# Kernel tuning notes

Measured on AMD Instinct MI355X. Metric: run time of the kernel, lower is better.

The kernel has to match this reference:

```python
import jax, jax.numpy as jnp
import numpy as np

B, T, C, H = 64, 256, 384, 6
HS = C // H  # 64


def _ln(x, w, b, eps=1e-5):
    m = jnp.mean(x, axis=-1, keepdims=True)
    v = jnp.mean((x - m) ** 2, axis=-1, keepdims=True)
    return (x - m) / jnp.sqrt(v + eps) * w + b


def setup_inputs() -> dict:
    key = jax.random.key(0)
    ks = jax.random.split(key, 18)
    sc = 0.02
    return {
        "x": jax.random.normal(ks[0], (B, T, C), jnp.float32),
        "ln1_w": jnp.ones((C,), jnp.float32),
        "ln1_b": jnp.zeros((C,), jnp.float32),
        # per-head Q/K/V linears stacked over the head axis: [H, C, HS]
        "Wq": jax.random.normal(ks[1], (H, C, HS), jnp.float32) * sc,
        "bq": jnp.zeros((H, HS), jnp.float32),
        "Wk": jax.random.normal(ks[2], (H, C, HS), jnp.float32) * sc,
        "bk": jnp.zeros((H, HS), jnp.float32),
        "Wv": jax.random.normal(ks[3], (H, C, HS), jnp.float32) * sc,
        "bv": jnp.zeros((H, HS), jnp.float32),
        "Wproj": jax.random.normal(ks[4], (C, C), jnp.float32) * sc,
        "bproj": jnp.zeros((C,), jnp.float32),
        "ln2_w": jnp.ones((C,), jnp.float32),
        "ln2_b": jnp.zeros((C,), jnp.float32),
        "W1": jax.random.normal(ks[5], (C, 4 * C), jnp.float32) * sc,
        "b1": jnp.zeros((4 * C,), jnp.float32),
        "W2": jax.random.normal(ks[6], (4 * C, C), jnp.float32) * sc,
        "b2": jnp.zeros((C,), jnp.float32),
    }


def reference(x, ln1_w, ln1_b, Wq, bq, Wk, bk, Wv, bv, Wproj, bproj,
              ln2_w, ln2_b, W1, b1, W2, b2):
    # --- pre-norm causal MHA (dropout = identity in eval) ---
    h = _ln(x, ln1_w, ln1_b)
    Q = jnp.einsum('btc,hcd->bhtd', h, Wq) + bq[None, :, None, :]
    K = jnp.einsum('btc,hcd->bhtd', h, Wk) + bk[None, :, None, :]
    V = jnp.einsum('btc,hcd->bhtd', h, Wv) + bv[None, :, None, :]
    scores = jnp.einsum('bhtd,bhsd->bhts', Q, K) * (HS ** -0.5)
    mask = jnp.tril(jnp.ones((x.shape[1], x.shape[1]), bool))
    scores = jnp.where(mask, scores, -jnp.inf)
    wei = jax.nn.softmax(scores, axis=-1)
    o = jnp.einsum('bhts,bhsd->bhtd', wei, V)
    # concat heads (same order as torch.cat over head list)
    o = o.transpose(0, 2, 1, 3).reshape(x.shape[0], x.shape[1], C)
    x1 = x + o @ Wproj + bproj
    # --- pre-norm FFN with exact (erf) GELU, matching torch default ---
    h2 = _ln(x1, ln2_w, ln2_b)
    f = jax.nn.gelu(h2 @ W1 + b1, approximate=False) @ W2 + b2
    return x1 + f
```

## Files before the change

### kernel.cpp

```cpp
#include <hip/hip_runtime.h>
#include <math.h>

constexpr int Bsz  = 64;
constexpr int Tseq = 256;
constexpr int Cdim = 384;
constexpr int Hh   = 6;
constexpr int HSd  = 64;
constexpr int Mrows = Bsz * Tseq;
constexpr int Cffn  = 4 * Cdim;
constexpr int Nqkv  = 3 * Cdim;

typedef __attribute__((ext_vector_type(8))) short short8;
typedef __attribute__((ext_vector_type(4))) float f32x4;

__device__ __forceinline__ ushort f2bf(float x) {
  union { float f; uint u; } a; a.f = x;
  uint r = a.u + 0x7fffu + ((a.u >> 16) & 1u);
  return (ushort)(r >> 16);
}
__device__ __forceinline__ float bf2f(ushort u) {
  union { uint u; float f; } a; a.u = ((uint)u) << 16;
  return a.f;
}

__device__ __forceinline__ float gelu_fast(float x) {
  float t = x * x;
  float u = x * fmaf(0.044715f, t, 1.0f);
  float e = fminf(1.5957691216f * u, 80.f);
  float z = __expf(e);
  return x * (z / (1.0f + z));
}

__global__ __launch_bounds__(256) void prep_kernel(
    const float* __restrict__ Wq, const float* __restrict__ Wk,
    const float* __restrict__ Wv, const float* __restrict__ Wproj,
    const float* __restrict__ W1, const float* __restrict__ W2,
    const float* __restrict__ bq, const float* __restrict__ bk,
    const float* __restrict__ bv,
    ushort* __restrict__ WqkvT, ushort* __restrict__ WprojT,
    ushort* __restrict__ W1T, ushort* __restrict__ W2T,
    float* __restrict__ bqkv) {
  const int bid = blockIdx.x;
  if (bid >= 1728) {
    int i = (bid - 1728) * 256 + threadIdx.x;
    if (i < Nqkv)
      bqkv[i] = (i < 384) ? bq[i] : (i < 768) ? bk[i - 384] : bv[i - 768];
    return;
  }
  const int tx = threadIdx.x & 31, ty = threadIdx.x >> 5;
  const float* src; ushort* dst; int R, S, r0, s0;
  if (bid < 432) {
    int which = bid / 144, rem = bid % 144;
    const float* W = (which == 0) ? Wq : (which == 1) ? Wk : Wv;
    int bz = rem / 24, t = rem % 24;
    R = 384; S = 64;
    src = W + (size_t)bz * R * S;
    dst = WqkvT + (size_t)which * 384 * 384 + (size_t)bz * R * S;
    r0 = (t >> 1) * 32; s0 = (t & 1) * 32;
  } else if (bid < 576) {
    int rem = bid - 432; R = 384; S = 384; src = Wproj; dst = WprojT;
    r0 = (rem / 12) * 32; s0 = (rem % 12) * 32;
  } else if (bid < 1152) {
    int rem = bid - 576; R = 384; S = 1536; src = W1; dst = W1T;
    r0 = (rem / 48) * 32; s0 = (rem % 48) * 32;
  } else {
    int rem = bid - 1152; R = 1536; S = 384; src = W2; dst = W2T;
    r0 = (rem / 12) * 32; s0 = (rem % 12) * 32;
  }
  __shared__ float t[32][33];
#pragma unroll
  for (int i = 0; i < 32; i += 8)
    t[ty + i][tx] = src[(size_t)(r0 + ty + i) * S + s0 + tx];
  __syncthreads();
#pragma unroll
  for (int i = 0; i < 32; i += 8)
    dst[(size_t)(s0 + ty + i) * R + r0 + tx] = f2bf(t[tx][ty + i]);
}

template <typename T>
__global__ __launch_bounds__(256) void ln_kernel(
    const T* __restrict__ x, const float* __restrict__ w,
    const float* __restrict__ b, ushort* __restrict__ out, int nrows) {
  int row  = blockIdx.x * 4 + (threadIdx.x >> 6);
  int lane = threadIdx.x & 63;
  if (row >= nrows) return;
  const T* xr = x + (size_t)row * Cdim;
  float v[6];
  float s = 0.f;
#pragma unroll
  for (int i = 0; i < 6; ++i) {
    if constexpr (sizeof(T) == 2) v[i] = bf2f(xr[lane + 64 * i]);
    else                          v[i] = xr[lane + 64 * i];
    s += v[i];
  }
#pragma unroll
  for (int off = 32; off > 0; off >>= 1) s += __shfl_xor(s, off, 64);
  float mean = s * (1.f / Cdim);
  float sq = 0.f;
#pragma unroll
  for (int i = 0; i < 6; ++i) { float d = v[i] - mean; sq += d * d; }
#pragma unroll
  for (int off = 32; off > 0; off >>= 1) sq += __shfl_xor(sq, off, 64);
  float rstd = rsqrtf(sq * (1.f / Cdim) + 1e-5f);
  ushort* orow = out + (size_t)row * Cdim;
#pragma unroll
  for (int i = 0; i < 6; ++i) {
    int c = lane + 64 * i;
    orow[c] = f2bf((v[i] - mean) * rstd * w[c] + b[c]);
  }
}

template <int EPI, int BN>
__global__ __launch_bounds__(256) void mfma_gemm(
    const ushort* __restrict__ A, const ushort* __restrict__ Bt,
    const float* __restrict__ bias, const void* __restrict__ res,
    void* __restrict__ Cout, void* __restrict__ C2, void* __restrict__ C3,
    int M, int N, int K) {
  constexpr int WC = BN / 2;
  constexpr int JN = WC / 16;
  constexpr int NB = BN / 32;
  __shared__ ushort Als[2 * 128 * 64];
  __shared__ ushort Bls[2 * BN * 64];
  const int tid = threadIdx.x;

  const int lid = blockIdx.y * gridDim.x + blockIdx.x;
  const int xcd = lid & 7, idx = lid >> 3;
  const int by = xcd * 16 + (idx & 15);
  const int bx = idx >> 4;
  const int m0 = by * 128, n0 = bx * BN;

  const int lane = tid & 63;
  const int w    = tid >> 6;
  const int wr   = (w >> 1) * 64;
  const int wc   = (w & 1) * WC;
  const int lm   = lane & 15;
  const int g    = lane >> 4;
  const int rq   = g * 4;

  const int wub = (tid & ~63) * 8;

  f32x4 acc[4][JN] = {};

  auto stage = [&](int k0, int bf) {
    ushort* Ab = Als + bf * (128 * 64);
    ushort* Bb = Bls + bf * (BN * 64);
#pragma unroll
    for (int q = 0; q < 4; ++q) {
      const int ci = tid + q * 256;
      const int row = ci >> 3;
      const int kc = ((ci & 7) ^ (row & 7)) * 8;
      const ushort* gA = A + (size_t)(m0 + row) * K + k0 + kc;
      __builtin_amdgcn_global_load_lds(
          (const __attribute__((address_space(1))) uint*)gA,
          (__attribute__((address_space(3))) uint*)(Ab + wub + q * 2048),
          16, 0, 0);
    }
#pragma unroll
    for (int q = 0; q < NB; ++q) {
      const int ci = tid + q * 256;
      const int row = ci >> 3;
      const int kc = ((ci & 7) ^ (row & 7)) * 8;
      const ushort* gB = Bt + (size_t)(n0 + row) * K + k0 + kc;
      __builtin_amdgcn_global_load_lds(
          (const __attribute__((address_space(1))) uint*)gB,
          (__attribute__((address_space(3))) uint*)(Bb + wub + q * 2048),
          16, 0, 0);
    }
  };

  const int nt = K >> 6;
  stage(0, 0);

  for (int t = 0, k0 = 0; t < nt; ++t, k0 += 64) {
    const int cur = t & 1;
    if (t + 1 < nt) {
      stage(k0 + 64, cur ^ 1);
      if constexpr (NB == 4)
        asm volatile("s_waitcnt vmcnt(8)" ::: "memory");
      else
        asm volatile("s_waitcnt vmcnt(6)" ::: "memory");
    } else {
      asm volatile("s_waitcnt vmcnt(0)" ::: "memory");
    }
    __builtin_amdgcn_sched_barrier(0);
    __builtin_amdgcn_s_barrier();
    __builtin_amdgcn_sched_barrier(0);

    const ushort* Ab = Als + cur * (128 * 64);
    const ushort* Bb = Bls + cur * (BN * 64);
#pragma unroll
    for (int half = 0; half < 2; ++half) {
      const int sl = ((half << 2) | g) ^ (lm & 7);
      short8 af[4], bfr[JN];
#pragma unroll
      for (int i = 0; i < 4; ++i)
        af[i] = *(const short8*)&Ab[(wr + i * 16 + lm) * 64 + sl * 8];
#pragma unroll
      for (int j = 0; j < JN; ++j)
        bfr[j] = *(const short8*)&Bb[(wc + j * 16 + lm) * 64 + sl * 8];
#pragma unroll
      for (int i = 0; i < 4; ++i)
#pragma unroll
        for (int j = 0; j < JN; ++j)
          acc[i][j] = __builtin_amdgcn_mfma_f32_16x16x32_bf16(af[i], bfr[j],
                                                              acc[i][j], 0, 0, 0);
    }

    asm volatile("s_waitcnt lgkmcnt(0)" ::: "memory");
    __builtin_amdgcn_sched_barrier(0);
    __builtin_amdgcn_s_barrier();
    __builtin_amdgcn_sched_barrier(0);
  }

  float bb[JN];
#pragma unroll
  for (int j = 0; j < JN; ++j) bb[j] = bias[n0 + wc + j * 16 + lm];

#pragma unroll
  for (int i = 0; i < 4; ++i) {
#pragma unroll
    for (int r = 0; r < 4; ++r) {
      const int row = m0 + wr + i * 16 + rq + r;
      if (EPI == 1) {
        const float* resrow = (const float*)res + (size_t)row * N + n0 + wc;
        ushort* crow = (ushort*)Cout + (size_t)row * N + n0 + wc;
#pragma unroll
        for (int j = 0; j < JN; ++j) {
          float rv = __builtin_nontemporal_load(resrow + j * 16 + lm);
          crow[j * 16 + lm] = f2bf(acc[i][j][r] + bb[j] + rv);
        }
      } else if (EPI == 4) {
        const ushort* resrow = (const ushort*)res + (size_t)row * N + n0 + wc;
        float* crow = (float*)Cout + (size_t)row * N + n0 + wc;
#pragma unroll
        for (int j = 0; j < JN; ++j)
          crow[j * 16 + lm] = acc[i][j][r] + bb[j] + bf2f(resrow[j * 16 + lm]);
      } else if (EPI == 3) {
        const int bb_ = row >> 8, tt = row & 255;
#pragma unroll
        for (int j = 0; j < JN; ++j) {
          const int colb = n0 + wc + j * 16;
          const int sec = colb / 384, cc = colb % 384;
          const int hh = cc >> 6, db = (cc & 63) + lm;
          ushort* dstp = (sec == 0) ? (ushort*)Cout
                       : (sec == 1) ? (ushort*)C2 : (ushort*)C3;
          dstp[((size_t)(bb_ * Hh + hh) * Tseq + tt) * HSd + db] =
              f2bf(acc[i][j][r] + bb[j]);
        }
      } else {
        ushort* crow = (ushort*)Cout + (size_t)row * N + n0 + wc;
#pragma unroll
        for (int j = 0; j < JN; ++j)
          crow[j * 16 + lm] = f2bf(gelu_fast(acc[i][j][r] + bb[j]));
      }
    }
  }
}

__global__ __launch_bounds__(256) void attn_kernel(
    const ushort* __restrict__ Qb, const ushort* __restrict__ Kb,
    const ushort* __restrict__ Vb, ushort* __restrict__ Oc) {
  __shared__ ushort Ks[64 * 72];
  __shared__ ushort Vt[64 * 72];
  __shared__ ushort Pl[4][16 * 72];
  const int bh = blockIdx.x, qt = blockIdx.y;
  const int b = bh / Hh, h = bh % Hh;
  const int tid = threadIdx.x;
  const int w = tid >> 6, lane = tid & 63;
  const int g = lane >> 4, n16 = lane & 15;

  const ushort* qrow = Qb + ((size_t)bh * Tseq + qt * 64 + w * 16 + n16) * HSd;
  short8 qf0 = *(const short8*)(qrow + g * 8);
  short8 qf1 = *(const short8*)(qrow + 32 + g * 8);

  f32x4 oacc[4] = {};
  float m_r[4], l_r[4];
#pragma unroll
  for (int r = 0; r < 4; ++r) { m_r[r] = -1e30f; l_r[r] = 0.f; }

  const int t0 = qt * 64 + w * 16 + g * 4;

  const ushort* Ksrc = Kb + (size_t)bh * Tseq * HSd;
  const ushort* Vsrc = Vb + (size_t)bh * Tseq * HSd;

  for (int st = 0; st <= qt; ++st) {
    __syncthreads();
    for (int c = tid; c < 512; c += 256) {
      int kr = c >> 3, kc = (c & 7) * 8;
      *(uint4*)&Ks[kr * 72 + kc] =
          *(const uint4*)&Ksrc[(size_t)(st * 64 + kr) * HSd + kc];
      int vr = c & 63, vc = (c >> 6) * 8;
      uint4 vv = *(const uint4*)&Vsrc[(size_t)(st * 64 + vr) * HSd + vc];
      const ushort* pv = (const ushort*)&vv;
#pragma unroll
      for (int i = 0; i < 8; ++i) Vt[(vc + i) * 72 + vr] = pv[i];
    }
    __syncthreads();

    f32x4 s[4];
#pragma unroll
    for (int ct = 0; ct < 4; ++ct) {
      short8 kf0 = *(const short8*)&Ks[(ct * 16 + n16) * 72 + g * 8];
      short8 kf1 = *(const short8*)&Ks[(ct * 16 + n16) * 72 + 32 + g * 8];
      f32x4 z = {};
      z = __builtin_amdgcn_mfma_f32_16x16x32_bf16(qf0, kf0, z, 0, 0, 0);
      z = __builtin_amdgcn_mfma_f32_16x16x32_bf16(qf1, kf1, z, 0, 0, 0);
      s[ct] = z;
    }

#pragma unroll
    for (int ct = 0; ct < 4; ++ct) {
      const int s_col = st * 64 + ct * 16 + n16;
#pragma unroll
      for (int r = 0; r < 4; ++r) {
        float v = s[ct][r] * 0.125f;
        s[ct][r] = (s_col > t0 + r) ? -1e30f : v;
      }
    }

#pragma unroll
    for (int r = 0; r < 4; ++r) {
      float m = fmaxf(fmaxf(s[0][r], s[1][r]), fmaxf(s[2][r], s[3][r]));
      m = fmaxf(m, __shfl_xor(m, 1, 64));
      m = fmaxf(m, __shfl_xor(m, 2, 64));
      m = fmaxf(m, __shfl_xor(m, 4, 64));
      m = fmaxf(m, __shfl_xor(m, 8, 64));
      float mnew = fmaxf(m_r[r], m);
      float alpha = __expf(m_r[r] - mnew);
      m_r[r] = mnew;
      float ssum = 0.f;
#pragma unroll
      for (int ct = 0; ct < 4; ++ct) {
        float p = __expf(s[ct][r] - mnew);
        s[ct][r] = p;
        ssum += p;
      }
      ssum += __shfl_xor(ssum, 1, 64);
      ssum += __shfl_xor(ssum, 2, 64);
      ssum += __shfl_xor(ssum, 4, 64);
      ssum += __shfl_xor(ssum, 8, 64);
      l_r[r] = l_r[r] * alpha + ssum;
#pragma unroll
      for (int j = 0; j < 4; ++j) oacc[j][r] *= alpha;
    }

    ushort* pw = &Pl[w][0];
#pragma unroll
    for (int ct = 0; ct < 4; ++ct)
#pragma unroll
      for (int r = 0; r < 4; ++r)
        pw[(g * 4 + r) * 72 + ct * 16 + n16] = f2bf(s[ct][r]);

    short8 pf0 = *(const short8*)&pw[n16 * 72 + g * 8];
    short8 pf1 = *(const short8*)&pw[n16 * 72 + 32 + g * 8];
#pragma unroll
    for (int j = 0; j < 4; ++j) {
      short8 vf0 = *(const short8*)&Vt[(j * 16 + n16) * 72 + g * 8];
      short8 vf1 = *(const short8*)&Vt[(j * 16 + n16) * 72 + 32 + g * 8];
      oacc[j] = __builtin_amdgcn_mfma_f32_16x16x32_bf16(pf0, vf0, oacc[j], 0, 0, 0);
      oacc[j] = __builtin_amdgcn_mfma_f32_16x16x32_bf16(pf1, vf1, oacc[j], 0, 0, 0);
    }
  }

  float inv[4];
#pragma unroll
  for (int r = 0; r < 4; ++r) inv[r] = 1.f / l_r[r];
  ushort* orow = Oc + ((size_t)(b * Tseq + qt * 64 + w * 16)) * Cdim + h * HSd;
#pragma unroll
  for (int j = 0; j < 4; ++j)
#pragma unroll
    for (int r = 0; r < 4; ++r)
      orow[(size_t)(g * 4 + r) * Cdim + j * 16 + n16] = f2bf(oacc[j][r] * inv[r]);
}

extern "C" void kernel_launch(void* const* d_in, const int* in_sizes, int n_in,
                              void* d_out, int out_size, void* d_ws, size_t ws_size,
                              hipStream_t stream) {
  const float* x      = (const float*)d_in[0];
  const float* ln1_w  = (const float*)d_in[1];
  const float* ln1_b  = (const float*)d_in[2];
  const float* Wq     = (const float*)d_in[3];
  const float* bq     = (const float*)d_in[4];
  const float* Wk     = (const float*)d_in[5];
  const float* bk     = (const float*)d_in[6];
  const float* Wv     = (const float*)d_in[7];
  const float* bv     = (const float*)d_in[8];
  const float* Wproj  = (const float*)d_in[9];
  const float* bproj  = (const float*)d_in[10];
  const float* ln2_w  = (const float*)d_in[11];
  const float* ln2_b  = (const float*)d_in[12];
  const float* W1     = (const float*)d_in[13];
  const float* b1     = (const float*)d_in[14];
  const float* W2     = (const float*)d_in[15];
  const float* b2     = (const float*)d_in[16];
  float* out = (float*)d_out;

  char* p = (char*)d_ws;
  ushort* h     = (ushort*)p;  p += (size_t)Mrows * Cdim * 2;
  ushort* Qb    = (ushort*)p;  p += (size_t)Mrows * Cdim * 2;
  ushort* Kb    = (ushort*)p;  p += (size_t)Mrows * Cdim * 2;
  ushort* Vb    = (ushort*)p;  p += (size_t)Mrows * Cdim * 2;
  ushort* Oc    = (ushort*)p;  p += (size_t)Mrows * Cdim * 2;
  ushort* g     = (ushort*)p;  p += (size_t)Mrows * Cffn * 2;
  ushort* WqkvT = (ushort*)p;  p += (size_t)Nqkv * Cdim * 2;
  ushort* WprojT= (ushort*)p;  p += (size_t)Cdim * Cdim * 2;
  ushort* W1T   = (ushort*)p;  p += (size_t)Cffn * Cdim * 2;
  ushort* W2T   = (ushort*)p;  p += (size_t)Cdim * Cffn * 2;
  float*  bqkv  = (float*)p;   p += (size_t)Nqkv * 4;
  ushort* h2 = h;
  ushort* x1 = Qb;

  dim3 blk(256);

  prep_kernel<<<dim3(1733), blk, 0, stream>>>(Wq, Wk, Wv, Wproj, W1, W2,
                                              bq, bk, bv,
                                              WqkvT, WprojT, W1T, W2T, bqkv);

  ln_kernel<float><<<dim3(Mrows / 4), blk, 0, stream>>>(x, ln1_w, ln1_b, h, Mrows);

  mfma_gemm<3, 128><<<dim3(Nqkv / 128, Mrows / 128), blk, 0, stream>>>(
      h, WqkvT, bqkv, nullptr, Qb, Kb, Vb, Mrows, Nqkv, Cdim);

  attn_kernel<<<dim3(Bsz * Hh, 4), blk, 0, stream>>>(Qb, Kb, Vb, Oc);

  mfma_gemm<1, 64><<<dim3(Cdim / 64, Mrows / 128), blk, 0, stream>>>(
      Oc, WprojT, bproj, x, x1, nullptr, nullptr, Mrows, Cdim, Cdim);

  ln_kernel<ushort><<<dim3(Mrows / 4), blk, 0, stream>>>(x1, ln2_w, ln2_b, h2, Mrows);

  mfma_gemm<2, 128><<<dim3(Cffn / 128, Mrows / 128), blk, 0, stream>>>(
      h2, W1T, b1, nullptr, g, nullptr, nullptr, Mrows, Cffn, Cdim);

  mfma_gemm<4, 64><<<dim3(Cdim / 64, Mrows / 128), blk, 0, stream>>>(
      g, W2T, b2, x1, out, nullptr, nullptr, Mrows, Cdim, Cffn);
}
```

Baseline: 245.4 us.

## Make GEMMs persistent and overlap each tile's epilogue with the next tile's loads

```diff
diff --git a/kernel.cpp b/kernel.cpp
--- a/kernel.cpp
+++ b/kernel.cpp
@@ -119,15 +119,10 @@
   constexpr int WC = BN / 2;
   constexpr int JN = WC / 16;
   constexpr int NB = BN / 32;
+  constexpr int LPT = 4 + NB;
   __shared__ ushort Als[2 * 128 * 64];
   __shared__ ushort Bls[2 * BN * 64];
   const int tid = threadIdx.x;
-
-  const int lid = blockIdx.y * gridDim.x + blockIdx.x;
-  const int xcd = lid & 7, idx = lid >> 3;
-  const int by = xcd * 16 + (idx & 15);
-  const int bx = idx >> 4;
-  const int m0 = by * 128, n0 = bx * BN;
 
   const int lane = tid & 63;
   const int w    = tid >> 6;
@@ -138,10 +133,11 @@
   const int rq   = g * 4;
 
   const int wub = (tid & ~63) * 8;
-
-  f32x4 acc[4][JN] = {};
-
-  auto stage = [&](int k0, int bf) {
+  const int nt  = K >> 6;
+  const int TT  = (N / BN) * (M / 128);
+  const int G   = gridDim.x;
+
+  auto stage = [&](int m0, int n0, int k0, int bf) {
     ushort* Ab = Als + bf * (128 * 64);
     ushort* Bb = Bls + bf * (BN * 64);
 #pragma unroll
@@ -168,93 +164,129 @@
     }
   };
 
-  const int nt = K >> 6;
-  stage(0, 0);
-
-  for (int t = 0, k0 = 0; t < nt; ++t, k0 += 64) {
-    const int cur = t & 1;
-    if (t + 1 < nt) {
-      stage(k0 + 64, cur ^ 1);
-      if constexpr (NB == 4)
-        asm volatile("s_waitcnt vmcnt(8)" ::: "memory");
-      else
-        asm volatile("s_waitcnt vmcnt(6)" ::: "memory");
-    } else {
-      asm volatile("s_waitcnt vmcnt(0)" ::: "memory");
-    }
+  f32x4 acc[4][JN];
+  float bb[JN];
+  int pm0 = 0, pn0 = 0;
+  bool havePrev = false;
+
+  auto epilogue = [&](int m0_, int n0_) {
+#pragma unroll
+    for (int i = 0; i < 4; ++i) {
+#pragma unroll
+      for (int r = 0; r < 4; ++r) {
+        const int row = m0_ + wr + i * 16 + rq + r;
+        if (EPI == 1) {
+          const float* resrow = (const float*)res + (size_t)row * N + n0_ + wc;
+          ushort* crow = (ushort*)Cout + (size_t)row * N + n0_ + wc;
+#pragma unroll
+          for (int j = 0; j < JN; ++j) {
+            float rv = __builtin_nontemporal_load(resrow + j * 16 + lm);
+            crow[j * 16 + lm] = f2bf(acc[i][j][r] + bb[j] + rv);
+          }
+        } else if (EPI == 4) {
+          const ushort* resrow = (const ushort*)res + (size_t)row * N + n0_ + wc;
+          float* crow = (float*)Cout + (size_t)row * N + n0_ + wc;
+#pragma unroll
+          for (int j = 0; j < JN; ++j)
+            crow[j * 16 + lm] = acc[i][j][r] + bb[j] + bf2f(resrow[j * 16 + lm]);
+        } else if (EPI == 3) {
+          const int bb_ = row >> 8, tt = row & 255;
+#pragma unroll
+          for (int j = 0; j < JN; ++j) {
+            const int colb = n0_ + wc + j * 16;
+            const int sec = colb / 384, cc = colb % 384;
+            const int hh = cc >> 6, db = (cc & 63) + lm;
+            ushort* dstp = (sec == 0) ? (ushort*)Cout
+                         : (sec == 1) ? (ushort*)C2 : (ushort*)C3;
+            dstp[((size_t)(bb_ * Hh + hh) * Tseq + tt) * HSd + db] =
+                f2bf(acc[i][j][r] + bb[j]);
+          }
+        } else {
+          ushort* crow = (ushort*)Cout + (size_t)row * N + n0_ + wc;
+#pragma unroll
+          for (int j = 0; j < JN; ++j)
+            crow[j * 16 + lm] = f2bf(gelu_fast(acc[i][j][r] + bb[j]));
+        }
+      }
+    }
+  };
+
+  for (int lid = blockIdx.x; lid < TT; lid += G) {
+    const int xcd = lid & 7, idx = lid >> 3;
+    const int by = xcd * 16 + (idx & 15);
+    const int bx = idx >> 4;
+    const int m0 = by * 128, n0 = bx * BN;
+
+    stage(m0, n0, 0, 0);
+    float nb[JN];
+#pragma unroll
+    for (int j = 0; j < JN; ++j) nb[j] = bias[n0 + wc + j * 16 + lm];
+    if (havePrev) epilogue(pm0, pn0);
+#pragma unroll
+    for (int j = 0; j < JN; ++j) bb[j] = nb[j];
+#pragma unroll
+    for (int i = 0; i < 4; ++i)
+#pragma unroll
+      for (int j = 0; j < JN; ++j) acc[i][j] = f32x4{0.f, 0.f, 0.f, 0.f};
+
+    stage(m0, n0, 64, 1);
+    if constexpr (LPT == 8)
+      asm volatile("s_waitcnt vmcnt(8)" ::: "memory");
+    else
+      asm volatile("s_waitcnt vmcnt(6)" ::: "memory");
     __builtin_amdgcn_sched_barrier(0);
     __builtin_amdgcn_s_barrier();
     __builtin_amdgcn_sched_barrier(0);
 
-    const ushort* Ab = Als + cur * (128 * 64);
-    const ushort* Bb = Bls + cur * (BN * 64);
-#pragma unroll
-    for (int half = 0; half < 2; ++half) {
-      const int sl = ((half << 2) | g) ^ (lm & 7);
-      short8 af[4], bfr[JN];
-#pragma unroll
-      for (int i = 0; i < 4; ++i)
-        af[i] = *(const short8*)&Ab[(wr + i * 16 + lm) * 64 + sl * 8];
-#pragma unroll
-      for (int j = 0; j < JN; ++j)
-        bfr[j] = *(const short8*)&Bb[(wc + j * 16 + lm) * 64 + sl * 8];
-#pragma unroll
-      for (int i = 0; i < 4; ++i)
+    for (int t = 0; t < nt; ++t) {
+      const int cur = t & 1;
+      const ushort* Ab = Als + cur * (128 * 64);
+      const ushort* Bb = Bls + cur * (BN * 64);
+#pragma unroll
+      for (int half = 0; half < 2; ++half) {
+        const int sl = ((half << 2) | g) ^ (lm & 7);
+        short8 af[4], bfr[JN];
+#pragma unroll
+        for (int i = 0; i < 4; ++i)
+          af[i] = *(const short8*)&Ab[(wr + i * 16 + lm) * 64 + sl * 8];
 #pragma unroll
         for (int j = 0; j < JN; ++j)
-          acc[i][j] = __builtin_amdgcn_mfma_f32_16x16x32_bf16(af[i], bfr[j],
-                                                              acc[i][j], 0, 0, 0);
-    }
-
-    asm volatile("s_waitcnt lgkmcnt(0)" ::: "memory");
-    __builtin_amdgcn_sched_barrier(0);
-    __builtin_amdgcn_s_barrier();
-    __builtin_amdgcn_sched_barrier(0);
-  }
-
-  float bb[JN];
-#pragma unroll
-  for (int j = 0; j < JN; ++j) bb[j] = bias[n0 + wc + j * 16 + lm];
-
-#pragma unroll
-  for (int i = 0; i < 4; ++i) {
-#pragma unroll
-    for (int r = 0; r < 4; ++r) {
-      const int row = m0 + wr + i * 16 + rq + r;
-      if (EPI == 1) {
-        const float* resrow = (const float*)res + (size_t)row * N + n0 + wc;
-        ushort* crow = (ushort*)Cout + (size_t)row * N + n0 + wc;
-#pragma unroll
-        for (int j = 0; j < JN; ++j) {
-          float rv = __builtin_nontemporal_load(resrow + j * 16 + lm);
-          crow[j * 16 + lm] = f2bf(acc[i][j][r] + bb[j] + rv);
+          bfr[j] = *(const short8*)&Bb[(wc + j * 16 + lm) * 64 + sl * 8];
+        __builtin_amdgcn_s_setprio(1);
+#pragma unroll
+        for (int i = 0; i < 4; ++i)
+#pragma unroll
+          for (int j = 0; j < JN; ++j)
+            acc[i][j] = __builtin_amdgcn_mfma_f32_16x16x32_bf16(
+                af[i], bfr[j], acc[i][j], 0, 0, 0);
+        __builtin_amdgcn_s_setprio(0);
+      }
+
+      asm volatile("s_waitcnt lgkmcnt(0)" ::: "memory");
+      __builtin_amdgcn_sched_barrier(0);
+      __builtin_amdgcn_s_barrier();
+      __builtin_amdgcn_sched_barrier(0);
+
+      if (t + 2 < nt) stage(m0, n0, (t + 2) * 64, cur);
+      if (t + 1 < nt) {
+        if (t + 2 < nt) {
+          if constexpr (LPT == 8)
+            asm volatile("s_waitcnt vmcnt(8)" ::: "memory");
+          else
+            asm volatile("s_waitcnt vmcnt(6)" ::: "memory");
+        } else {
+          asm volatile("s_waitcnt vmcnt(0)" ::: "memory");
         }
-      } else if (EPI == 4) {
-        const ushort* resrow = (const ushort*)res + (size_t)row * N + n0 + wc;
-        float* crow = (float*)Cout + (size_t)row * N + n0 + wc;
-#pragma unroll
-        for (int j = 0; j < JN; ++j)
-          crow[j * 16 + lm] = acc[i][j][r] + bb[j] + bf2f(resrow[j * 16 + lm]);
-      } else if (EPI == 3) {
-        const int bb_ = row >> 8, tt = row & 255;
-#pragma unroll
-        for (int j = 0; j < JN; ++j) {
-          const int colb = n0 + wc + j * 16;
-          const int sec = colb / 384, cc = colb % 384;
-          const int hh = cc >> 6, db = (cc & 63) + lm;
-          ushort* dstp = (sec == 0) ? (ushort*)Cout
-                       : (sec == 1) ? (ushort*)C2 : (ushort*)C3;
-          dstp[((size_t)(bb_ * Hh + hh) * Tseq + tt) * HSd + db] =
-              f2bf(acc[i][j][r] + bb[j]);
-        }
-      } else {
-        ushort* crow = (ushort*)Cout + (size_t)row * N + n0 + wc;
-#pragma unroll
-        for (int j = 0; j < JN; ++j)
-          crow[j * 16 + lm] = f2bf(gelu_fast(acc[i][j][r] + bb[j]));
+        __builtin_amdgcn_sched_barrier(0);
+        __builtin_amdgcn_s_barrier();
+        __builtin_amdgcn_sched_barrier(0);
       }
     }
-  }
+
+    pm0 = m0; pn0 = n0; havePrev = true;
+  }
+
+  if (havePrev) epilogue(pm0, pn0);
 }
 
 __global__ __launch_bounds__(256) void attn_kernel(
@@ -418,19 +450,19 @@
 
   ln_kernel<float><<<dim3(Mrows / 4), blk, 0, stream>>>(x, ln1_w, ln1_b, h, Mrows);
 
-  mfma_gemm<3, 128><<<dim3(Nqkv / 128, Mrows / 128), blk, 0, stream>>>(
+  mfma_gemm<3, 128><<<dim3(512), blk, 0, stream>>>(
       h, WqkvT, bqkv, nullptr, Qb, Kb, Vb, Mrows, Nqkv, Cdim);
 
   attn_kernel<<<dim3(Bsz * Hh, 4), blk, 0, stream>>>(Qb, Kb, Vb, Oc);
 
-  mfma_gemm<1, 64><<<dim3(Cdim / 64, Mrows / 128), blk, 0, stream>>>(
+  mfma_gemm<1, 64><<<dim3(768), blk, 0, stream>>>(
       Oc, WprojT, bproj, x, x1, nullptr, nullptr, Mrows, Cdim, Cdim);
 
   ln_kernel<ushort><<<dim3(Mrows / 4), blk, 0, stream>>>(x1, ln2_w, ln2_b, h2, Mrows);
 
-  mfma_gemm<2, 128><<<dim3(Cffn / 128, Mrows / 128), blk, 0, stream>>>(
+  mfma_gemm<2, 128><<<dim3(512), blk, 0, stream>>>(
       h2, W1T, b1, nullptr, g, nullptr, nullptr, Mrows, Cffn, Cdim);
 
-  mfma_gemm<4, 64><<<dim3(Cdim / 64, Mrows / 128), blk, 0, stream>>>(
+  mfma_gemm<4, 64><<<dim3(768), blk, 0, stream>>>(
       g, W2T, b2, x1, out, nullptr, nullptr, Mrows, Cdim, Cffn);
 }
```

New measurement: 554.8 us. +126.1%, slower.

## Permute GEMM output columns for packed bf16 stores and fold permutation into weights

Applied to the files above, without the earlier changes.

```diff
diff --git a/kernel.cpp b/kernel.cpp
--- a/kernel.cpp
+++ b/kernel.cpp
@@ -21,6 +21,11 @@
 __device__ __forceinline__ float bf2f(ushort u) {
   union { uint u; float f; } a; a.u = ((uint)u) << 16;
   return a.f;
+}
+__device__ __forceinline__ uint pk_bf16(float lo, float hi) {
+  uint r;
+  asm("v_cvt_pk_bf16_f32 %0, %1, %2" : "=v"(r) : "v"(lo), "v"(hi));
+  return r;
 }
 
 __device__ __forceinline__ float gelu_fast(float x) {
@@ -48,7 +53,7 @@
     return;
   }
   const int tx = threadIdx.x & 31, ty = threadIdx.x >> 5;
-  const float* src; ushort* dst; int R, S, r0, s0;
+  const float* src; ushort* dst; int R, S, r0, s0, perm = 0;
   if (bid < 432) {
     int which = bid / 144, rem = bid % 144;
     const float* W = (which == 0) ? Wq : (which == 1) ? Wk : Wv;
@@ -59,22 +64,26 @@
     r0 = (t >> 1) * 32; s0 = (t & 1) * 32;
   } else if (bid < 576) {
     int rem = bid - 432; R = 384; S = 384; src = Wproj; dst = WprojT;
-    r0 = (rem / 12) * 32; s0 = (rem % 12) * 32;
+    r0 = (rem / 12) * 32; s0 = (rem % 12) * 32; perm = 1;
   } else if (bid < 1152) {
     int rem = bid - 576; R = 384; S = 1536; src = W1; dst = W1T;
     r0 = (rem / 48) * 32; s0 = (rem % 48) * 32;
   } else {
     int rem = bid - 1152; R = 1536; S = 384; src = W2; dst = W2T;
-    r0 = (rem / 12) * 32; s0 = (rem % 12) * 32;
+    r0 = (rem / 12) * 32; s0 = (rem % 12) * 32; perm = 2;
   }
   __shared__ float t[32][33];
 #pragma unroll
   for (int i = 0; i < 32; i += 8)
     t[ty + i][tx] = src[(size_t)(r0 + ty + i) * S + s0 + tx];
   __syncthreads();
+  const int kk = r0 + tx;
+  int kp = kk;
+  if (perm == 1) kp = (kk & ~63) | (((kk & 15) << 2) | ((kk >> 4) & 3));
+  else if (perm == 2) kp = (kk & 15) * 96 + (kk >> 4);
 #pragma unroll
   for (int i = 0; i < 32; i += 8)
-    dst[(size_t)(s0 + ty + i) * R + r0 + tx] = f2bf(t[tx][ty + i]);
+    dst[(size_t)(s0 + ty + i) * R + kp] = f2bf(t[tx][ty + i]);
 }
 
 template <typename T>
@@ -171,10 +180,10 @@
   const int nt = K >> 6;
   stage(0, 0);
 
-  for (int t = 0, k0 = 0; t < nt; ++t, k0 += 64) {
+  for (int t = 0; t < nt; ++t) {
     const int cur = t & 1;
     if (t + 1 < nt) {
-      stage(k0 + 64, cur ^ 1);
+      stage((t + 1) * 64, cur ^ 1);
       if constexpr (NB == 4)
         asm volatile("s_waitcnt vmcnt(8)" ::: "memory");
       else
@@ -198,12 +207,14 @@
 #pragma unroll
       for (int j = 0; j < JN; ++j)
         bfr[j] = *(const short8*)&Bb[(wc + j * 16 + lm) * 64 + sl * 8];
+      __builtin_amdgcn_s_setprio(1);
 #pragma unroll
       for (int i = 0; i < 4; ++i)
 #pragma unroll
         for (int j = 0; j < JN; ++j)
           acc[i][j] = __builtin_amdgcn_mfma_f32_16x16x32_bf16(af[i], bfr[j],
                                                               acc[i][j], 0, 0, 0);
+      __builtin_amdgcn_s_setprio(0);
     }
 
     asm volatile("s_waitcnt lgkmcnt(0)" ::: "memory");
@@ -221,7 +232,7 @@
 #pragma unroll
     for (int r = 0; r < 4; ++r) {
       const int row = m0 + wr + i * 16 + rq + r;
-      if (EPI == 1) {
+      if constexpr (EPI == 1) {
         const float* resrow = (const float*)res + (size_t)row * N + n0 + wc;
         ushort* crow = (ushort*)Cout + (size_t)row * N + n0 + wc;
 #pragma unroll
@@ -229,37 +240,35 @@
           float rv = __builtin_nontemporal_load(resrow + j * 16 + lm);
           crow[j * 16 + lm] = f2bf(acc[i][j][r] + bb[j] + rv);
         }
-      } else if (EPI == 4) {
+      } else if constexpr (EPI == 4) {
         const ushort* resrow = (const ushort*)res + (size_t)row * N + n0 + wc;
         float* crow = (float*)Cout + (size_t)row * N + n0 + wc;
 #pragma unroll
         for (int j = 0; j < JN; ++j)
           crow[j * 16 + lm] = acc[i][j][r] + bb[j] + bf2f(resrow[j * 16 + lm]);
-      } else if (EPI == 3) {
-        const int bb_ = row >> 8, tt = row & 255;
-#pragma unroll
-        for (int j = 0; j < JN; ++j) {
-          const int colb = n0 + wc + j * 16;
-          const int sec = colb / 384, cc = colb % 384;
-          const int hh = cc >> 6, db = (cc & 63) + lm;
-          ushort* dstp = (sec == 0) ? (ushort*)Cout
-                       : (sec == 1) ? (ushort*)C2 : (ushort*)C3;
-          dstp[((size_t)(bb_ * Hh + hh) * Tseq + tt) * HSd + db] =
-              f2bf(acc[i][j][r] + bb[j]);
-        }
+      } else if constexpr (EPI == 3) {
+        ushort* crow = (ushort*)Cout + (size_t)row * N + n0 + wc + lm * 4;
+        uint d0 = pk_bf16(acc[i][0][r] + bb[0], acc[i][1][r] + bb[1]);
+        uint d1 = pk_bf16(acc[i][2][r] + bb[2], acc[i][3][r] + bb[3]);
+        uint2 pkv; pkv.x = d0; pkv.y = d1;
+        *(uint2*)crow = pkv;
       } else {
-        ushort* crow = (ushort*)Cout + (size_t)row * N + n0 + wc;
-#pragma unroll
-        for (int j = 0; j < JN; ++j)
-          crow[j * 16 + lm] = f2bf(gelu_fast(acc[i][j][r] + bb[j]));
+        ushort* crow = (ushort*)Cout + (size_t)row * N + lm * 96 + ((n0 + wc) >> 4);
+        float g0 = gelu_fast(acc[i][0][r] + bb[0]);
+        float g1 = gelu_fast(acc[i][1][r] + bb[1]);
+        float g2 = gelu_fast(acc[i][2][r] + bb[2]);
+        float g3 = gelu_fast(acc[i][3][r] + bb[3]);
+        uint d0 = pk_bf16(g0, g1);
+        uint d1 = pk_bf16(g2, g3);
+        uint2 pkv; pkv.x = d0; pkv.y = d1;
+        *(uint2*)crow = pkv;
       }
     }
   }
 }
 
 __global__ __launch_bounds__(256) void attn_kernel(
-    const ushort* __restrict__ Qb, const ushort* __restrict__ Kb,
-    const ushort* __restrict__ Vb, ushort* __restrict__ Oc) {
+    const ushort* __restrict__ QKV, ushort* __restrict__ Oc) {
   __shared__ ushort Ks[64 * 72];
   __shared__ ushort Vt[64 * 72];
   __shared__ ushort Pl[4][16 * 72];
@@ -269,7 +278,8 @@
   const int w = tid >> 6, lane = tid & 63;
   const int g = lane >> 4, n16 = lane & 15;
 
-  const ushort* qrow = Qb + ((size_t)bh * Tseq + qt * 64 + w * 16 + n16) * HSd;
+  const ushort* qrow =
+      QKV + (size_t)(b * Tseq + qt * 64 + w * 16 + n16) * Nqkv + h * HSd;
   short8 qf0 = *(const short8*)(qrow + g * 8);
   short8 qf1 = *(const short8*)(qrow + 32 + g * 8);
 
@@ -280,17 +290,17 @@
 
   const int t0 = qt * 64 + w * 16 + g * 4;
 
-  const ushort* Ksrc = Kb + (size_t)bh * Tseq * HSd;
-  const ushort* Vsrc = Vb + (size_t)bh * Tseq * HSd;
+  const ushort* Ksrc = QKV + (size_t)b * Tseq * Nqkv + Cdim + h * HSd;
+  const ushort* Vsrc = QKV + (size_t)b * Tseq * Nqkv + 2 * Cdim + h * HSd;
 
   for (int st = 0; st <= qt; ++st) {
     __syncthreads();
     for (int c = tid; c < 512; c += 256) {
       int kr = c >> 3, kc = (c & 7) * 8;
       *(uint4*)&Ks[kr * 72 + kc] =
-          *(const uint4*)&Ksrc[(size_t)(st * 64 + kr) * HSd + kc];
+          *(const uint4*)&Ksrc[(size_t)(st * 64 + kr) * Nqkv + kc];
       int vr = c & 63, vc = (c >> 6) * 8;
-      uint4 vv = *(const uint4*)&Vsrc[(size_t)(st * 64 + vr) * HSd + vc];
+      uint4 vv = *(const uint4*)&Vsrc[(size_t)(st * 64 + vr) * Nqkv + vc];
       const ushort* pv = (const ushort*)&vv;
 #pragma unroll
       for (int i = 0; i < 8; ++i) Vt[(vc + i) * 72 + vr] = pv[i];
@@ -397,9 +407,7 @@
 
   char* p = (char*)d_ws;
   ushort* h     = (ushort*)p;  p += (size_t)Mrows * Cdim * 2;
-  ushort* Qb    = (ushort*)p;  p += (size_t)Mrows * Cdim * 2;
-  ushort* Kb    = (ushort*)p;  p += (size_t)Mrows * Cdim * 2;
-  ushort* Vb    = (ushort*)p;  p += (size_t)Mrows * Cdim * 2;
+  ushort* QKV   = (ushort*)p;  p += (size_t)Mrows * Nqkv * 2;
   ushort* Oc    = (ushort*)p;  p += (size_t)Mrows * Cdim * 2;
   ushort* g     = (ushort*)p;  p += (size_t)Mrows * Cffn * 2;
   ushort* WqkvT = (ushort*)p;  p += (size_t)Nqkv * Cdim * 2;
@@ -408,7 +416,7 @@
   ushort* W2T   = (ushort*)p;  p += (size_t)Cdim * Cffn * 2;
   float*  bqkv  = (float*)p;   p += (size_t)Nqkv * 4;
   ushort* h2 = h;
-  ushort* x1 = Qb;
+  ushort* x1 = QKV;
 
   dim3 blk(256);
 
@@ -419,9 +427,9 @@
   ln_kernel<float><<<dim3(Mrows / 4), blk, 0, stream>>>(x, ln1_w, ln1_b, h, Mrows);
 
   mfma_gemm<3, 128><<<dim3(Nqkv / 128, Mrows / 128), blk, 0, stream>>>(
-      h, WqkvT, bqkv, nullptr, Qb, Kb, Vb, Mrows, Nqkv, Cdim);
-
-  attn_kernel<<<dim3(Bsz * Hh, 4), blk, 0, stream>>>(Qb, Kb, Vb, Oc);
+      h, WqkvT, bqkv, nullptr, QKV, nullptr, nullptr, Mrows, Nqkv, Cdim);
+
+  attn_kernel<<<dim3(Bsz * Hh, 4), blk, 0, stream>>>(QKV, Oc);
 
   mfma_gemm<1, 64><<<dim3(Cdim / 64, Mrows / 128), blk, 0, stream>>>(
       Oc, WprojT, bproj, x, x1, nullptr, nullptr, Mrows, Cdim, Cdim);
```

Measured after the change: 258.2 us. +5.2%, slower.
